# Kernel tuning notes

Measured on AMD Instinct MI355X. Metric: run time of the kernel, lower is better.

Reference implementation:

```python
import jax, jax.numpy as jnp
import numpy as np

B, T, D = 2, 2048, 1024
NH = 16
HD = D // NH


def setup_inputs() -> dict:
    key = jax.random.key(0)
    ks = jax.random.split(key, 5)
    s = 0.02
    return {
        "x": jax.random.normal(ks[0], (B, T, D), dtype=jnp.float32),
        "Wq": jax.random.normal(ks[1], (D, D), dtype=jnp.float32) * s,
        "Wk": jax.random.normal(ks[2], (D, D), dtype=jnp.float32) * s,
        "Wv": jax.random.normal(ks[3], (D, D), dtype=jnp.float32) * s,
        "Wo": jax.random.normal(ks[4], (D, D), dtype=jnp.float32) * s,
        "bo": jnp.zeros((D,), dtype=jnp.float32),
    }


def reference(x, Wq, Wk, Wv, Wo, bo):
    b, t, _ = x.shape
    scale = HD ** -0.5
    # torch Linear: y = x @ W^T
    q = (x @ Wq.T).reshape(b, t, NH, HD)
    k = (x @ Wk.T).reshape(b, t, NH, HD)
    v = (x @ Wv.T).reshape(b, t, NH, HD)
    # scores: [b, nh, t, t]
    s = jnp.einsum("bqhd,bkhd->bhqk", q, k) * scale
    causal = jnp.tril(jnp.ones((t, t), dtype=bool))
    s = jnp.where(causal, s, -jnp.inf)
    p = jax.nn.softmax(s, axis=-1)
    o = jnp.einsum("bhqk,bkhd->bqhd", p, v).reshape(b, t, D)
    return o @ Wo.T + bo
```

## Files before the change

### kernel.cpp

```cpp
#include <hip/hip_runtime.h>


typedef __bf16 bf16x8 __attribute__((ext_vector_type(8)));
typedef float f32x4 __attribute__((ext_vector_type(4)));
typedef unsigned short ushortx8 __attribute__((ext_vector_type(8)));
typedef unsigned short ushortx4 __attribute__((ext_vector_type(4)));

#define T_SEQ 2048
#define NHEAD 16
#define HDIM 64
#define DMODEL 1024

__device__ inline unsigned short f2bf(float f) {
  unsigned int u = __builtin_bit_cast(unsigned int, f);
  unsigned int r = (u + 0x7fffu + ((u >> 16) & 1u)) >> 16;
  return (unsigned short)r;
}

__device__ inline void gl16(const unsigned short* g, unsigned short* l) {
  __builtin_amdgcn_global_load_lds(
      (const __attribute__((address_space(1))) unsigned int*)g,
      (__attribute__((address_space(3))) unsigned int*)l, 16, 0, 0);
}

__global__ void cast_all(const float* __restrict__ x, const float* __restrict__ w0,
                         const float* __restrict__ w1, const float* __restrict__ w2,
                         const float* __restrict__ w3, unsigned short* __restrict__ out) {
  const int NX = 2 * T_SEQ * DMODEL;
  int i = (blockIdx.x * 256 + threadIdx.x) * 4;
  const float* src;
  int off;
  if (i < NX) {
    src = x; off = i;
  } else {
    const int j = i - NX;
    const int sel = j >> 20;
    off = j & ((1 << 20) - 1);
    src = sel == 0 ? w0 : sel == 1 ? w1 : sel == 2 ? w2 : w3;
  }
  float4 v = *reinterpret_cast<const float4*>(src + off);
  ushortx4 o;
  o[0] = f2bf(v.x); o[1] = f2bf(v.y); o[2] = f2bf(v.z); o[3] = f2bf(v.w);
  *reinterpret_cast<ushortx4*>(out + i) = o;
}

__device__ __forceinline__ void gemm_core(
    const unsigned short* __restrict__ A, const unsigned short* __restrict__ Bw,
    int K, int m0, int n0, f32x4 acc[4][4]) {
  __shared__ unsigned short As[4096];
  __shared__ unsigned short Bs[4096];
  const int tid = threadIdx.x;
  const int lane = tid & 63, wid = tid >> 6;
  const int wr = wid >> 1, wc = wid & 1;
  const int lr = lane & 15, lg = lane >> 4;
  const int srow = tid >> 2;
  const int scs = ((tid & 3) ^ (srow & 3)) * 8;
  const unsigned short* ga0 = A + (size_t)(m0 + srow) * K + scs;
  const unsigned short* gb0 = Bw + (size_t)(n0 + srow) * K + scs;
  unsigned short* la0 = As + tid * 8;
  unsigned short* lb0 = Bs + tid * 8;
  const int rca = (lg ^ (lr & 3)) * 8;

  for (int k0 = 0; k0 < K; k0 += 32) {
    __syncthreads();
    gl16(ga0 + k0, la0);
    gl16(ga0 + (size_t)64 * K + k0, la0 + 2048);
    gl16(gb0 + k0, lb0);
    gl16(gb0 + (size_t)64 * K + k0, lb0 + 2048);
    __syncthreads();

    bf16x8 af[4], bfr[4];
#pragma unroll
    for (int t = 0; t < 4; ++t) {
      af[t]  = *reinterpret_cast<const bf16x8*>(&As[(wr * 64 + t * 16 + lr) * 32 + rca]);
      bfr[t] = *reinterpret_cast<const bf16x8*>(&Bs[(wc * 64 + t * 16 + lr) * 32 + rca]);
    }
#pragma unroll
    for (int mi = 0; mi < 4; ++mi)
#pragma unroll
      for (int ni = 0; ni < 4; ++ni)
        acc[mi][ni] = __builtin_amdgcn_mfma_f32_16x16x32_bf16(af[mi], bfr[ni], acc[mi][ni], 0, 0, 0);
  }
}

__global__ __launch_bounds__(256) void gemm_qkv(
    const unsigned short* __restrict__ xb, const unsigned short* __restrict__ Wall,
    unsigned short* __restrict__ Qb, unsigned short* __restrict__ Kb,
    unsigned short* __restrict__ Vtb) {
  const int z = blockIdx.y;
  const int bid = blockIdx.x;
  int m0, n0;
  const unsigned short* A;
  const unsigned short* Bw;
  if (z < 2) {
    n0 = (bid & 7) * 128; m0 = (bid >> 3) * 128;
    A = xb; Bw = Wall + (size_t)z * (DMODEL * DMODEL);
  } else {
    m0 = (bid & 7) * 128; n0 = (bid >> 3) * 128;
    A = Wall + (size_t)2 * (DMODEL * DMODEL); Bw = xb;
  }
  f32x4 acc[4][4] = {};
  gemm_core(A, Bw, DMODEL, m0, n0, acc);

  const int tid = threadIdx.x, lane = tid & 63, wid = tid >> 6;
  const int wr = wid >> 1, wc = wid & 1, lr = lane & 15, lg = lane >> 4;
  const int mb = m0 + wr * 64, nb = n0 + wc * 64;
  const float scale = z == 0 ? 0.125f * 1.44269504089f : 1.0f;
#pragma unroll
  for (int mi = 0; mi < 4; ++mi)
#pragma unroll
    for (int ni = 0; ni < 4; ++ni) {
      const int col = nb + ni * 16 + lr;
#pragma unroll
      for (int j = 0; j < 4; ++j) {
        const int row = mb + mi * 16 + lg * 4 + j;
        const float v = acc[mi][ni][j] * scale;
        if (z < 2) {
          const int b = row >> 11, t = row & (T_SEQ - 1);
          const int h = col >> 6, d = col & (HDIM - 1);
          unsigned short* out = z == 0 ? Qb : Kb;
          out[(((size_t)(b * NHEAD + h) * T_SEQ + t) << 6) + d] = f2bf(v);
        } else {
          const int h = row >> 6, d = row & (HDIM - 1);
          const int b = col >> 11, t = col & (T_SEQ - 1);
          Vtb[(((size_t)(b * NHEAD + h) * HDIM + d) << 11) + t] = f2bf(v);
        }
      }
    }
}

__global__ __launch_bounds__(256) void gemm_proj(
    const unsigned short* __restrict__ Ob, const unsigned short* __restrict__ Wob,
    float* __restrict__ out, const float* __restrict__ bias) {
  const int m0 = blockIdx.y * 128, n0 = blockIdx.x * 128;
  f32x4 acc[4][4] = {};
  gemm_core(Ob, Wob, DMODEL, m0, n0, acc);

  const int tid = threadIdx.x, lane = tid & 63, wid = tid >> 6;
  const int wr = wid >> 1, wc = wid & 1, lr = lane & 15, lg = lane >> 4;
  const int mb = m0 + wr * 64, nb = n0 + wc * 64;
#pragma unroll
  for (int mi = 0; mi < 4; ++mi)
#pragma unroll
    for (int ni = 0; ni < 4; ++ni) {
      const int col = nb + ni * 16 + lr;
      const float bv = bias[col];
#pragma unroll
      for (int j = 0; j < 4; ++j) {
        const int row = mb + mi * 16 + lg * 4 + j;
        out[(size_t)row * DMODEL + col] = acc[mi][ni][j] + bv;
      }
    }
}

__global__ __launch_bounds__(512, 4) void flash_attn(
    const unsigned short* __restrict__ Q, const unsigned short* __restrict__ Kg,
    const unsigned short* __restrict__ Vt, unsigned short* __restrict__ O) {
  __shared__ unsigned short Ks[4][4096];
  __shared__ unsigned short Vs[4][4096];
  const int tid = threadIdx.x, lane = tid & 63, wid = tid >> 6;
  const int lr = lane & 15, lg = lane >> 4;
  const int bid = blockIdx.x;
  const int bh = (bid & 7) * 4 + ((bid >> 3) & 3);
  const int a = (bid >> 5) & 15;
  const int btile = 31 - a;
  const int myq = (wid < 4) ? a : btile;
  const int qg = myq * 64 + (wid & 3) * 16;
  const size_t base = (size_t)bh * (T_SEQ * HDIM);
  const int q = qg + lr;

  bf16x8 qf[2];
#pragma unroll
  for (int h = 0; h < 2; ++h)
    qf[h] = *reinterpret_cast<const bf16x8*>(Q + base + (size_t)(qg + lr) * HDIM + h * 32 + lg * 8);
  asm volatile("s_waitcnt vmcnt(0)" ::: "memory");

  const int srow = tid >> 3;
  const int schk = ((tid & 7) ^ (srow & 7)) * 8;
  const unsigned short* kst = Kg + base + (size_t)srow * HDIM + schk;
  const unsigned short* vst = Vt + base + (size_t)srow * T_SEQ + schk;

#define STAGE(buf, kt_)                                \
  do {                                                 \
    const int kb_ = (kt_) * 64;                        \
    gl16(kst + (size_t)kb_ * HDIM, &Ks[buf][tid * 8]); \
    gl16(vst + kb_, &Vs[buf][tid * 8]);                \
  } while (0)

  int koff[4][2];
#pragma unroll
  for (int c = 0; c < 4; ++c)
#pragma unroll
    for (int h = 0; h < 2; ++h)
      koff[c][h] = (c * 16 + lr) * 64 + (((h * 4 + lg) ^ (lr & 7)) * 8);
  int voff[4][2][2];
#pragma unroll
  for (int dt = 0; dt < 4; ++dt)
#pragma unroll
    for (int ks = 0; ks < 2; ++ks) {
      const int g0 = (ks * 4 + (lg >> 1)) ^ (lr & 7);
      const int g1 = (ks * 4 + 2 + (lg >> 1)) ^ (lr & 7);
      voff[dt][ks][0] = (dt * 16 + lr) * 64 + g0 * 8 + (lg & 1) * 4;
      voff[dt][ks][1] = (dt * 16 + lr) * 64 + g1 * 8 + (lg & 1) * 4;
    }

  float mrun = -INFINITY, lrun = 0.f;
  f32x4 acc[4] = {};
  const int nt = btile + 1;

  STAGE(0, 0);
  STAGE(1, 1);
  STAGE(2, 2);

  for (int kt = 0; kt < nt; ++kt) {
    const int cb = kt & 3;
    const int ahead = btile - kt;
    if (ahead >= 3) {
      STAGE((kt + 3) & 3, kt + 3);
      asm volatile("s_waitcnt vmcnt(6)" ::: "memory");
    } else if (ahead == 2) {
      asm volatile("s_waitcnt vmcnt(4)" ::: "memory");
    } else if (ahead == 1) {
      asm volatile("s_waitcnt vmcnt(2)" ::: "memory");
    } else {
      asm volatile("s_waitcnt vmcnt(0)" ::: "memory");
    }
    __builtin_amdgcn_s_barrier();
    asm volatile("" ::: "memory");

    if (kt <= myq) {
      const int kb = kt * 64;
      f32x4 s[4] = {};
      bf16x8 kf[4][2];
#pragma unroll
      for (int c = 0; c < 4; ++c)
#pragma unroll
        for (int h = 0; h < 2; ++h)
          kf[c][h] = *reinterpret_cast<const bf16x8*>(&Ks[cb][koff[c][h]]);
#pragma unroll
      for (int c = 0; c < 4; ++c)
#pragma unroll
        for (int h = 0; h < 2; ++h)
          s[c] = __builtin_amdgcn_mfma_f32_16x16x32_bf16(kf[c][h], qf[h], s[c], 0, 0, 0);

      if (kt == myq) {
#pragma unroll
        for (int c = 0; c < 4; ++c)
#pragma unroll
          for (int j = 0; j < 4; ++j) {
            const int k = kb + c * 16 + lg * 4 + j;
            if (k > q) s[c][j] = -INFINITY;
          }
      }
      float tm = -INFINITY;
#pragma unroll
      for (int c = 0; c < 4; ++c)
#pragma unroll
        for (int j = 0; j < 4; ++j) tm = fmaxf(tm, s[c][j]);
      tm = fmaxf(tm, __shfl_xor(tm, 16, 64));
      tm = fmaxf(tm, __shfl_xor(tm, 32, 64));
      if (!__all(tm <= mrun + 8.f)) {
        const float mnew = fmaxf(mrun, tm);
        const float fac = exp2f(mrun - mnew);
        lrun *= fac;
#pragma unroll
        for (int dt = 0; dt < 4; ++dt)
#pragma unroll
          for (int j = 0; j < 4; ++j) acc[dt][j] *= fac;
        mrun = mnew;
      }
      float tsum = 0.f;
#pragma unroll
      for (int c = 0; c < 4; ++c)
#pragma unroll
        for (int j = 0; j < 4; ++j) {
          const float p = exp2f(s[c][j] - mrun);
          s[c][j] = p;
          tsum += p;
        }
      tsum += __shfl_xor(tsum, 16, 64);
      tsum += __shfl_xor(tsum, 32, 64);
      lrun += tsum;

      bf16x8 pb[2];
#pragma unroll
      for (int ks = 0; ks < 2; ++ks) {
        bf16x8 t8;
#pragma unroll
        for (int e = 0; e < 8; ++e) t8[e] = (__bf16)s[ks * 2 + (e >> 2)][e & 3];
        pb[ks] = t8;
      }
#pragma unroll
      for (int dt = 0; dt < 4; ++dt) {
#pragma unroll
        for (int ks = 0; ks < 2; ++ks) {
          uint2 vlo = *reinterpret_cast<const uint2*>(&Vs[cb][voff[dt][ks][0]]);
          uint2 vhi = *reinterpret_cast<const uint2*>(&Vs[cb][voff[dt][ks][1]]);
          uint4 u;
          u.x = vlo.x; u.y = vlo.y; u.z = vhi.x; u.w = vhi.y;
          bf16x8 vf = __builtin_bit_cast(bf16x8, u);
          acc[dt] = __builtin_amdgcn_mfma_f32_16x16x32_bf16(vf, pb[ks], acc[dt], 0, 0, 0);
        }
      }
    }
    asm volatile("" ::: "memory");
    __builtin_amdgcn_s_barrier();
  }
#undef STAGE

  const int b = bh >> 4, h = bh & (NHEAD - 1);
  const float inv = 1.0f / lrun;
  unsigned short* orow = O + (((size_t)(b * T_SEQ + q)) << 10) + h * HDIM + lg * 4;
#pragma unroll
  for (int dt = 0; dt < 4; ++dt) {
    ushortx4 o4;
#pragma unroll
    for (int j = 0; j < 4; ++j) o4[j] = f2bf(acc[dt][j] * inv);
    *reinterpret_cast<ushortx4*>(orow + dt * 16) = o4;
  }
}

extern "C" void kernel_launch(void* const* d_in, const int* in_sizes, int n_in,
                              void* d_out, int out_size, void* d_ws, size_t ws_size,
                              hipStream_t stream) {
  const float* x  = (const float*)d_in[0];
  const float* Wq = (const float*)d_in[1];
  const float* Wk = (const float*)d_in[2];
  const float* Wv = (const float*)d_in[3];
  const float* Wo = (const float*)d_in[4];
  const float* bo = (const float*)d_in[5];
  float* out = (float*)d_out;

  const int M = 2 * T_SEQ;
  const int NXD = DMODEL * DMODEL;
  const int NX = M * DMODEL;

  unsigned short* ws = (unsigned short*)d_ws;
  unsigned short* xb  = ws;
  unsigned short* Wqb = xb + NX;
  unsigned short* Wob = Wqb + 3 * (size_t)NXD;
  unsigned short* Qb  = Wqb + 4 * (size_t)NXD;
  unsigned short* Kbf = Qb + NX;
  unsigned short* Vtb = Kbf + NX;
  unsigned short* Ob  = Vtb + NX;

  cast_all<<<(NX + 4 * NXD) / 1024, 256, 0, stream>>>(x, Wq, Wk, Wv, Wo, xb);

  dim3 gq(256, 3);
  gemm_qkv<<<gq, 256, 0, stream>>>(xb, Wqb, Qb, Kbf, Vtb);

  flash_attn<<<512, 512, 0, stream>>>(Qb, Kbf, Vtb, Ob);

  dim3 gg(DMODEL / 128, M / 128);
  gemm_proj<<<gg, 256, 0, stream>>>(Ob, Wob, out, bo);
}
```

Before: 117.0 us.

## Split remaining diagonal-tile KV iterations across both wave groups and merge via LDS

Each block pairs a short query tile with a long one. Previously the four waves on the short tile sat idle while the other four finished the long tile. Now, once the short tile is done, both wave groups work on the long tile: one group takes even KV tiles and the other odd ones. Their partial softmax states (max, sum, accumulator) are then combined through shared memory. The prefetch schedule is rewritten to stage one to two tiles ahead with a full vmcnt(0) wait each step, which may expose more load latency. s_setprio is also wrapped around the MFMA sections.

Result: faster. 113.0 us (-3.5%).

```diff
diff --git a/kernel.cpp b/kernel.cpp
--- a/kernel.cpp
+++ b/kernel.cpp
@@ -153,169 +153,199 @@
     }
 }
 
+__device__ __forceinline__ void attn_step(
+    const unsigned short* Kslot, const unsigned short* Vslot,
+    const int kh0, const int kh1, const int (&vo)[2][2],
+    const bf16x8 (&qf)[2], f32x4 (&acc)[4], float& mrun, float& lrun,
+    const bool domask, const int kb, const int q, const int lg) {
+  f32x4 s[4] = {};
+  __builtin_amdgcn_s_setprio(1);
+#pragma unroll
+  for (int c = 0; c < 4; ++c) {
+    bf16x8 k0 = *reinterpret_cast<const bf16x8*>(&Kslot[kh0 + c * 1024]);
+    bf16x8 k1 = *reinterpret_cast<const bf16x8*>(&Kslot[kh1 + c * 1024]);
+    s[c] = __builtin_amdgcn_mfma_f32_16x16x32_bf16(k0, qf[0], s[c], 0, 0, 0);
+    s[c] = __builtin_amdgcn_mfma_f32_16x16x32_bf16(k1, qf[1], s[c], 0, 0, 0);
+  }
+  __builtin_amdgcn_s_setprio(0);
+  if (domask) {
+#pragma unroll
+    for (int c = 0; c < 4; ++c)
+#pragma unroll
+      for (int j = 0; j < 4; ++j) {
+        const int k = kb + c * 16 + lg * 4 + j;
+        if (k > q) s[c][j] = -INFINITY;
+      }
+  }
+  float tm = -INFINITY;
+#pragma unroll
+  for (int c = 0; c < 4; ++c)
+#pragma unroll
+    for (int j = 0; j < 4; ++j) tm = fmaxf(tm, s[c][j]);
+  tm = fmaxf(tm, __shfl_xor(tm, 16, 64));
+  tm = fmaxf(tm, __shfl_xor(tm, 32, 64));
+  if (!__all(tm <= mrun + 8.f)) {
+    const float mnew = fmaxf(mrun, tm);
+    const float fac = exp2f(mrun - mnew);
+    lrun *= fac;
+#pragma unroll
+    for (int dt = 0; dt < 4; ++dt)
+#pragma unroll
+      for (int j = 0; j < 4; ++j) acc[dt][j] *= fac;
+    mrun = mnew;
+  }
+  float tsum = 0.f;
+#pragma unroll
+  for (int c = 0; c < 4; ++c)
+#pragma unroll
+    for (int j = 0; j < 4; ++j) {
+      const float p = exp2f(s[c][j] - mrun);
+      s[c][j] = p;
+      tsum += p;
+    }
+  tsum += __shfl_xor(tsum, 16, 64);
+  tsum += __shfl_xor(tsum, 32, 64);
+  lrun += tsum;
+
+  bf16x8 pb[2];
+#pragma unroll
+  for (int ks = 0; ks < 2; ++ks) {
+    bf16x8 t8;
+#pragma unroll
+    for (int e = 0; e < 8; ++e) t8[e] = (__bf16)s[ks * 2 + (e >> 2)][e & 3];
+    pb[ks] = t8;
+  }
+  __builtin_amdgcn_s_setprio(1);
+#pragma unroll
+  for (int dt = 0; dt < 4; ++dt) {
+#pragma unroll
+    for (int ks = 0; ks < 2; ++ks) {
+      uint2 vlo = *reinterpret_cast<const uint2*>(&Vslot[vo[ks][0] + dt * 1024]);
+      uint2 vhi = *reinterpret_cast<const uint2*>(&Vslot[vo[ks][1] + dt * 1024]);
+      uint4 u;
+      u.x = vlo.x; u.y = vlo.y; u.z = vhi.x; u.w = vhi.y;
+      bf16x8 vf = __builtin_bit_cast(bf16x8, u);
+      acc[dt] = __builtin_amdgcn_mfma_f32_16x16x32_bf16(vf, pb[ks], acc[dt], 0, 0, 0);
+    }
+  }
+  __builtin_amdgcn_s_setprio(0);
+}
+
 __global__ __launch_bounds__(512, 4) void flash_attn(
     const unsigned short* __restrict__ Q, const unsigned short* __restrict__ Kg,
     const unsigned short* __restrict__ Vt, unsigned short* __restrict__ O) {
   __shared__ unsigned short Ks[4][4096];
   __shared__ unsigned short Vs[4][4096];
   const int tid = threadIdx.x, lane = tid & 63, wid = tid >> 6;
-  const int lr = lane & 15, lg = lane >> 4;
+  const int lr = lane & 15, lg = lane >> 4, wq = wid & 3;
   const int bid = blockIdx.x;
   const int bh = (bid & 7) * 4 + ((bid >> 3) & 3);
   const int a = (bid >> 5) & 15;
-  const int btile = 31 - a;
-  const int myq = (wid < 4) ? a : btile;
-  const int qg = myq * 64 + (wid & 3) * 16;
+  const int b = 31 - a;
+  const bool g0 = wid < 4;
+  const int myq1 = g0 ? a : b;
+  const int q1 = myq1 * 64 + wq * 16 + lr;
+  const int q2 = b * 64 + wq * 16 + lr;
   const size_t base = (size_t)bh * (T_SEQ * HDIM);
-  const int q = qg + lr;
-
-  bf16x8 qf[2];
-#pragma unroll
-  for (int h = 0; h < 2; ++h)
-    qf[h] = *reinterpret_cast<const bf16x8*>(Q + base + (size_t)(qg + lr) * HDIM + h * 32 + lg * 8);
-  asm volatile("s_waitcnt vmcnt(0)" ::: "memory");
+
+  bf16x8 qf1[2], qf2[2];
+#pragma unroll
+  for (int h = 0; h < 2; ++h) {
+    qf1[h] = *reinterpret_cast<const bf16x8*>(Q + base + (size_t)q1 * HDIM + h * 32 + lg * 8);
+    qf2[h] = *reinterpret_cast<const bf16x8*>(Q + base + (size_t)q2 * HDIM + h * 32 + lg * 8);
+  }
 
   const int srow = tid >> 3;
   const int schk = ((tid & 7) ^ (srow & 7)) * 8;
   const unsigned short* kst = Kg + base + (size_t)srow * HDIM + schk;
   const unsigned short* vst = Vt + base + (size_t)srow * T_SEQ + schk;
 
-#define STAGE(buf, kt_)                                \
-  do {                                                 \
-    const int kb_ = (kt_) * 64;                        \
-    gl16(kst + (size_t)kb_ * HDIM, &Ks[buf][tid * 8]); \
-    gl16(vst + kb_, &Vs[buf][tid * 8]);                \
+#define STAGE(slot, kt_)                                \
+  do {                                                  \
+    const int kb_ = (kt_) * 64;                         \
+    gl16(kst + (size_t)kb_ * HDIM, &Ks[slot][tid * 8]); \
+    gl16(vst + kb_, &Vs[slot][tid * 8]);                \
   } while (0)
 
-  int koff[4][2];
-#pragma unroll
-  for (int c = 0; c < 4; ++c)
-#pragma unroll
-    for (int h = 0; h < 2; ++h)
-      koff[c][h] = (c * 16 + lr) * 64 + (((h * 4 + lg) ^ (lr & 7)) * 8);
-  int voff[4][2][2];
-#pragma unroll
-  for (int dt = 0; dt < 4; ++dt)
-#pragma unroll
-    for (int ks = 0; ks < 2; ++ks) {
-      const int g0 = (ks * 4 + (lg >> 1)) ^ (lr & 7);
-      const int g1 = (ks * 4 + 2 + (lg >> 1)) ^ (lr & 7);
-      voff[dt][ks][0] = (dt * 16 + lr) * 64 + g0 * 8 + (lg & 1) * 4;
-      voff[dt][ks][1] = (dt * 16 + lr) * 64 + g1 * 8 + (lg & 1) * 4;
-    }
-
-  float mrun = -INFINITY, lrun = 0.f;
-  f32x4 acc[4] = {};
-  const int nt = btile + 1;
+  const int kh0 = lr * 64 + (((0 * 4 + lg) ^ (lr & 7)) * 8);
+  const int kh1 = lr * 64 + (((1 * 4 + lg) ^ (lr & 7)) * 8);
+  int vo[2][2];
+#pragma unroll
+  for (int ks = 0; ks < 2; ++ks) {
+    vo[ks][0] = lr * 64 + (((ks * 4 + (lg >> 1)) ^ (lr & 7)) * 8) + (lg & 1) * 4;
+    vo[ks][1] = lr * 64 + (((ks * 4 + 2 + (lg >> 1)) ^ (lr & 7)) * 8) + (lg & 1) * 4;
+  }
+
+  float m1 = -INFINITY, l1 = 0.f, m2 = -INFINITY, l2 = 0.f;
+  f32x4 acc1[4] = {}, acc2[4] = {};
 
   STAGE(0, 0);
-  STAGE(1, 1);
-  STAGE(2, 2);
-
-  for (int kt = 0; kt < nt; ++kt) {
-    const int cb = kt & 3;
-    const int ahead = btile - kt;
-    if (ahead >= 3) {
-      STAGE((kt + 3) & 3, kt + 3);
-      asm volatile("s_waitcnt vmcnt(6)" ::: "memory");
-    } else if (ahead == 2) {
-      asm volatile("s_waitcnt vmcnt(4)" ::: "memory");
-    } else if (ahead == 1) {
-      asm volatile("s_waitcnt vmcnt(2)" ::: "memory");
+  asm volatile("s_waitcnt vmcnt(0)" ::: "memory");
+  __builtin_amdgcn_s_barrier();
+  asm volatile("" ::: "memory");
+
+  for (int kt = 0; kt <= a; ++kt) {
+    if (kt < a) {
+      STAGE((kt + 1) & 3, kt + 1);
     } else {
-      asm volatile("s_waitcnt vmcnt(0)" ::: "memory");
-    }
+      STAGE((a + 1) & 3, a + 1);
+      if (a + 2 <= b) STAGE((a + 2) & 3, a + 2);
+    }
+    attn_step(Ks[kt & 3], Vs[kt & 3], kh0, kh1, vo, qf1, acc1, m1, l1,
+              g0 && (kt == a), kt * 64, q1, lg);
+    asm volatile("s_waitcnt vmcnt(0)" ::: "memory");
     __builtin_amdgcn_s_barrier();
     asm volatile("" ::: "memory");
-
-    if (kt <= myq) {
-      const int kb = kt * 64;
-      f32x4 s[4] = {};
-      bf16x8 kf[4][2];
-#pragma unroll
-      for (int c = 0; c < 4; ++c)
-#pragma unroll
-        for (int h = 0; h < 2; ++h)
-          kf[c][h] = *reinterpret_cast<const bf16x8*>(&Ks[cb][koff[c][h]]);
-#pragma unroll
-      for (int c = 0; c < 4; ++c)
-#pragma unroll
-        for (int h = 0; h < 2; ++h)
-          s[c] = __builtin_amdgcn_mfma_f32_16x16x32_bf16(kf[c][h], qf[h], s[c], 0, 0, 0);
-
-      if (kt == myq) {
-#pragma unroll
-        for (int c = 0; c < 4; ++c)
-#pragma unroll
-          for (int j = 0; j < 4; ++j) {
-            const int k = kb + c * 16 + lg * 4 + j;
-            if (k > q) s[c][j] = -INFINITY;
-          }
-      }
-      float tm = -INFINITY;
-#pragma unroll
-      for (int c = 0; c < 4; ++c)
-#pragma unroll
-        for (int j = 0; j < 4; ++j) tm = fmaxf(tm, s[c][j]);
-      tm = fmaxf(tm, __shfl_xor(tm, 16, 64));
-      tm = fmaxf(tm, __shfl_xor(tm, 32, 64));
-      if (!__all(tm <= mrun + 8.f)) {
-        const float mnew = fmaxf(mrun, tm);
-        const float fac = exp2f(mrun - mnew);
-        lrun *= fac;
-#pragma unroll
-        for (int dt = 0; dt < 4; ++dt)
-#pragma unroll
-          for (int j = 0; j < 4; ++j) acc[dt][j] *= fac;
-        mrun = mnew;
-      }
-      float tsum = 0.f;
-#pragma unroll
-      for (int c = 0; c < 4; ++c)
-#pragma unroll
-        for (int j = 0; j < 4; ++j) {
-          const float p = exp2f(s[c][j] - mrun);
-          s[c][j] = p;
-          tsum += p;
-        }
-      tsum += __shfl_xor(tsum, 16, 64);
-      tsum += __shfl_xor(tsum, 32, 64);
-      lrun += tsum;
-
-      bf16x8 pb[2];
-#pragma unroll
-      for (int ks = 0; ks < 2; ++ks) {
-        bf16x8 t8;
-#pragma unroll
-        for (int e = 0; e < 8; ++e) t8[e] = (__bf16)s[ks * 2 + (e >> 2)][e & 3];
-        pb[ks] = t8;
-      }
-#pragma unroll
-      for (int dt = 0; dt < 4; ++dt) {
-#pragma unroll
-        for (int ks = 0; ks < 2; ++ks) {
-          uint2 vlo = *reinterpret_cast<const uint2*>(&Vs[cb][voff[dt][ks][0]]);
-          uint2 vhi = *reinterpret_cast<const uint2*>(&Vs[cb][voff[dt][ks][1]]);
-          uint4 u;
-          u.x = vlo.x; u.y = vlo.y; u.z = vhi.x; u.w = vhi.y;
-          bf16x8 vf = __builtin_bit_cast(bf16x8, u);
-          acc[dt] = __builtin_amdgcn_mfma_f32_16x16x32_bf16(vf, pb[ks], acc[dt], 0, 0, 0);
-        }
-      }
-    }
+  }
+
+  for (int t0 = a + 1; t0 <= b; t0 += 2) {
+    if (t0 + 2 <= b) STAGE((t0 + 2) & 3, t0 + 2);
+    if (t0 + 3 <= b) STAGE((t0 + 3) & 3, t0 + 3);
+    if (!g0) {
+      attn_step(Ks[t0 & 3], Vs[t0 & 3], kh0, kh1, vo, qf2, acc1, m1, l1,
+                t0 == b, t0 * 64, q2, lg);
+    } else if (t0 + 1 <= b) {
+      attn_step(Ks[(t0 + 1) & 3], Vs[(t0 + 1) & 3], kh0, kh1, vo, qf2, acc2, m2, l2,
+                false, (t0 + 1) * 64, q2, lg);
+    }
+    asm volatile("s_waitcnt vmcnt(0)" ::: "memory");
+    __builtin_amdgcn_s_barrier();
     asm volatile("" ::: "memory");
-    __builtin_amdgcn_s_barrier();
   }
 #undef STAGE
 
-  const int b = bh >> 4, h = bh & (NHEAD - 1);
-  const float inv = 1.0f / lrun;
-  unsigned short* orow = O + (((size_t)(b * T_SEQ + q)) << 10) + h * HDIM + lg * 4;
+  float* sm = reinterpret_cast<float*>(&Ks[0][0]);
+  const int lid = (wq * 64 + lane) * 18;
+  if (g0) {
+    float* p = sm + lid;
+    p[0] = m2; p[1] = l2;
+#pragma unroll
+    for (int dt = 0; dt < 4; ++dt)
+#pragma unroll
+      for (int j = 0; j < 4; ++j) p[2 + dt * 4 + j] = acc2[dt][j];
+  }
+  __syncthreads();
+  if (!g0) {
+    const float* p = sm + lid;
+    const float mo = p[0], lo = p[1];
+    const float ms = fmaxf(m1, mo);
+    const float f1 = exp2f(m1 - ms), f2 = exp2f(mo - ms);
+    l1 = l1 * f1 + lo * f2;
+#pragma unroll
+    for (int dt = 0; dt < 4; ++dt)
+#pragma unroll
+      for (int j = 0; j < 4; ++j)
+        acc1[dt][j] = acc1[dt][j] * f1 + p[2 + dt * 4 + j] * f2;
+  }
+
+  const int b_ = bh >> 4, h_ = bh & (NHEAD - 1);
+  const float inv = 1.0f / l1;
+  unsigned short* orow = O + (((size_t)(b_ * T_SEQ + q1)) << 10) + h_ * HDIM + lg * 4;
 #pragma unroll
   for (int dt = 0; dt < 4; ++dt) {
     ushortx4 o4;
 #pragma unroll
-    for (int j = 0; j < 4; ++j) o4[j] = f2bf(acc[dt][j] * inv);
+    for (int j = 0; j < 4; ++j) o4[j] = f2bf(acc1[dt][j] * inv);
     *reinterpret_cast<ushortx4*>(orow + dt * 16) = o4;
   }
 }
```
